# Kernel tuning notes

Measured on AMD Instinct MI355X. Metric: run time of the kernel, lower is better.

## Reference

```python
import jax, jax.numpy as jnp
import numpy as np

N_NODES = 50000
N_EDGES = 400000
D = 100  # trans_units = node_dim = edge_dim = out_dim


def setup_inputs() -> dict:
    key = jax.random.key(0)
    ks = jax.random.split(key, 8)
    x = jax.random.normal(ks[0], (N_NODES, D), dtype=jnp.float32)
    edge_h = jax.random.normal(ks[1], (N_EDGES, D), dtype=jnp.float32)
    src = jax.random.randint(ks[2], (N_EDGES,), 0, N_NODES)
    dst = jax.random.randint(ks[3], (N_EDGES,), 0, N_NODES)
    # xavier-normal-ish init scales (gain for relu ~ sqrt(2))
    W_fc = jax.random.normal(ks[4], (D, D), dtype=jnp.float32) * np.sqrt(2.0 / (D + D))
    W_rel = jax.random.normal(ks[5], (2 * D, D), dtype=jnp.float32) * np.sqrt(2.0 / (3 * D))
    b_rel = jnp.zeros((D,), dtype=jnp.float32)
    W_attn = jax.random.normal(ks[6], (2 * D, 1), dtype=jnp.float32) * np.sqrt(2.0 / (2 * D + 1))
    return {"x": x, "edge_h": edge_h, "src": src, "dst": dst,
            "W_fc": W_fc, "W_rel": W_rel, "b_rel": b_rel, "W_attn": W_attn}


def reference(x, edge_h, src, dst, W_fc, W_rel, b_rel, W_attn):
    """RGATLayer forward (single layer, single head, as in RGAT defaults).

    z = fc(x); per-edge: end = relation_fc([edge_h, z[dst]]);
    e = leaky_relu(attn_fc([z[src], end])); alpha = softmax over incoming
    edges of each dst node; h[dst] = sum alpha * z[src].
    """
    n = x.shape[0]
    z = x @ W_fc                                              # [N, D]
    z_src = z[src]                                            # [E, D]
    z_dst = z[dst]                                            # [E, D]
    end = jnp.concatenate([edge_h, z_dst], axis=-1) @ W_rel + b_rel   # [E, D]
    a = jnp.concatenate([z_src, end], axis=-1) @ W_attn              # [E, 1]
    e = jax.nn.leaky_relu(a[:, 0], negative_slope=0.01)             # [E]
    # segment softmax over edges grouped by destination node
    m = jax.ops.segment_max(e, dst, num_segments=n)                  # [N]
    ex = jnp.exp(e - m[dst])                                         # [E]
    denom = jax.ops.segment_sum(ex, dst, num_segments=n)            # [N]
    alpha = ex / denom[dst]                                          # [E]
    # weighted scatter-sum of source messages (zero-in-degree nodes -> 0)
    h = jax.ops.segment_sum(alpha[:, None] * z_src, dst, num_segments=n)  # [N, D]
    return h
```

## Files before the change

### kernel.cpp

```cpp
#include <hip/hip_runtime.h>
#include <hip/hip_bf16.h>

#define NN 50000
#define NE 400000
#define DD 100
#define CAP 32

#define OFF_P    0
#define OFF_Q    112
#define OFF_C    224
#define OFF_WB   240
#define OFF_S    7424
#define OFF_T    (OFF_S + NN)
#define OFF_CNT  (OFF_T + NN)
#define OFF_PAY  (OFF_CNT + NN + 16)
#define OFF_Z    (OFF_PAY + 2 * CAP * NN)

#define FC_ROWS 128
#define NFCB ((NN + FC_ROWS - 1) / FC_ROWS)

#define PB_FOLD 51
#define PB_ZERO 49
#define PB_WPK  4

typedef __attribute__((ext_vector_type(8))) short bf8;
typedef __attribute__((ext_vector_type(4))) float f4;

__device__ __forceinline__ unsigned pk2(float a, float b) {
    __hip_bfloat16 ha = __float2bfloat16(a), hb = __float2bfloat16(b);
    unsigned short ua, ub;
    __builtin_memcpy(&ua, &ha, 2); __builtin_memcpy(&ub, &hb, 2);
    return (unsigned)ua | ((unsigned)ub << 16);
}
__device__ __forceinline__ float bflo(unsigned u) { return __uint_as_float(u << 16); }
__device__ __forceinline__ float bfhi(unsigned u) { return __uint_as_float(u & 0xffff0000u); }

__global__ void k_prep(const float* __restrict__ W_rel, const float* __restrict__ b_rel,
                       const float* __restrict__ W_attn, const float* __restrict__ W_fc,
                       float* __restrict__ ws) {
    int b = blockIdx.x, t = threadIdx.x;
    const int lane = t & 63;
    if (b < PB_FOLD) {
        int gw = b * 4 + (t >> 6);
        if (gw < 201) {
            const float* row = (gw < 200) ? (W_rel + (size_t)gw * DD) : b_rel;
            float v0 = (lane < DD)      ? W_attn[DD + lane]      : 0.f;
            float v1 = (lane + 64 < DD) ? W_attn[DD + 64 + lane] : 0.f;
            float a0 = (lane < DD)      ? row[lane]      : 0.f;
            float a1 = (lane + 64 < DD) ? row[64 + lane] : 0.f;
            float s = fmaf(a0, v0, a1 * v1);
            #pragma unroll
            for (int m = 1; m < 64; m <<= 1) s += __shfl_xor(s, m);
            if (lane == 0) {
                if (gw < 100)      ws[OFF_P + gw] = s;
                else if (gw < 200) ws[OFF_Q + gw - 100] = s;
                else               ws[OFF_C] = s;
            }
        }
    } else if (b < PB_FOLD + PB_ZERO) {
        int* cnt = (int*)(ws + OFF_CNT);
        int i0 = (b - PB_FOLD) * 1024 + t;
        int lim = (b - PB_FOLD) * 1024 + 1024; if (lim > NN) lim = NN;
        for (int i = i0; i < lim; i += 256) cnt[i] = 0;
    } else {
        char* wbB = (char*)(ws + OFF_WB);
        int bi = b - PB_FOLD - PB_ZERO;
        for (int i = bi * 1792 + t; i < (bi + 1) * 1792; i += 256) {
            int kp = i / 112, c = i - kp * 112;
            int k = 2 * kp;
            float f0 = (c < DD && k < DD)     ? W_fc[k * DD + c]       : 0.f;
            float f1 = (c < DD && k + 1 < DD) ? W_fc[(k + 1) * DD + c] : 0.f;
            int sw = (c & 7) << 4;
            *(unsigned*)(wbB + ((c * 256 + 2 * k) ^ sw)) = pk2(f0, f1);
        }
    }
}

__launch_bounds__(256, 4)
__global__ void k_fc(const float* __restrict__ x, const float* __restrict__ W_attn,
                     float* __restrict__ ws) {
    __shared__ __align__(16) char smem[32768];
    int tid = threadIdx.x;

    int row0 = blockIdx.x * FC_ROWS;
    int nrows = NN - row0; if (nrows > FC_ROWS) nrows = FC_ROWS;

    char* xb = smem;
    const float4* x4 = reinterpret_cast<const float4*>(x + (size_t)row0 * DD);
    for (int i = tid; i < 128 * 25; i += 256) {
        int r = i / 25, k4 = i - r * 25, k = k4 * 4;
        float4 v = (r < nrows) ? x4[i] : make_float4(0.f, 0.f, 0.f, 0.f);
        int sw = (r & 7) << 4;
        *(unsigned*)(xb + ((r * 256 + 2 * k) ^ sw))     = pk2(v.x, v.y);
        *(unsigned*)(xb + ((r * 256 + 2 * k + 4) ^ sw)) = pk2(v.z, v.w);
    }
    for (int i = tid; i < 128 * 7; i += 256) {
        int r = i / 7, j = i - r * 7, k = 100 + j * 4;
        int sw = (r & 7) << 4;
        *(unsigned*)(xb + ((r * 256 + 2 * k) ^ sw)) = 0u;
        *(unsigned*)(xb + ((r * 256 + 2 * k + 4) ^ sw)) = 0u;
    }
    __syncthreads();

    const int w = tid >> 6, lane = tid & 63;
    const int lq = lane & 15, lg = lane >> 4;
    const int sw = (lq & 7) << 4;
    const char* wbG = (const char*)(ws + OFF_WB);

    f4 acc[2][7];
    #pragma unroll
    for (int mt = 0; mt < 2; ++mt)
        #pragma unroll
        for (int nt = 0; nt < 7; ++nt)
            acc[mt][nt] = (f4){0.f, 0.f, 0.f, 0.f};

    #pragma unroll
    for (int ks = 0; ks < 4; ++ks) {
        const int ko = ks * 64 + lg * 16;
        bf8 a0 = *(const bf8*)(xb + (((w * 32 + lq) * 256 + ko) ^ sw));
        bf8 a1 = *(const bf8*)(xb + (((w * 32 + 16 + lq) * 256 + ko) ^ sw));
        #pragma unroll
        for (int nt = 0; nt < 7; ++nt) {
            bf8 bfr = *(const bf8*)(wbG + (((nt * 16 + lq) * 256 + ko) ^ sw));
            acc[0][nt] = __builtin_amdgcn_mfma_f32_16x16x32_bf16(a0, bfr, acc[0][nt], 0, 0, 0);
            acc[1][nt] = __builtin_amdgcn_mfma_f32_16x16x32_bf16(a1, bfr, acc[1][nt], 0, 0, 0);
        }
    }

    float sp0[4] = {0,0,0,0}, sp1[4] = {0,0,0,0}, tp0[4] = {0,0,0,0}, tp1[4] = {0,0,0,0};
    #pragma unroll
    for (int nt = 0; nt < 7; ++nt) {
        int col = nt * 16 + lq;
        float uv = W_attn[col];
        float qv = ws[OFF_Q + col];
        #pragma unroll
        for (int r = 0; r < 4; ++r) {
            sp0[r] = fmaf(acc[0][nt][r], uv, sp0[r]);
            tp0[r] = fmaf(acc[0][nt][r], qv, tp0[r]);
            sp1[r] = fmaf(acc[1][nt][r], uv, sp1[r]);
            tp1[r] = fmaf(acc[1][nt][r], qv, tp1[r]);
        }
    }
    #pragma unroll
    for (int m = 1; m < 16; m <<= 1) {
        #pragma unroll
        for (int r = 0; r < 4; ++r) {
            sp0[r] += __shfl_xor(sp0[r], m);
            tp0[r] += __shfl_xor(tp0[r], m);
            sp1[r] += __shfl_xor(sp1[r], m);
            tp1[r] += __shfl_xor(tp1[r], m);
        }
    }
    if (lq == 0) {
        #pragma unroll
        for (int r = 0; r < 4; ++r) {
            int g0 = row0 + w * 32 + lg * 4 + r;
            int g1 = g0 + 16;
            if (g0 < NN) { ws[OFF_S + g0] = sp0[r]; ws[OFF_T + g0] = tp0[r]; }
            if (g1 < NN) { ws[OFF_S + g1] = sp1[r]; ws[OFF_T + g1] = tp1[r]; }
        }
    }

    __syncthreads();
    float* zt = (float*)smem;
    #pragma unroll
    for (int half = 0; half < 2; ++half) {
        if ((w >> 1) == half) {
            #pragma unroll
            for (int mt = 0; mt < 2; ++mt)
                #pragma unroll
                for (int nt = 0; nt < 7; ++nt) {
                    int c = nt * 16 + lq;
                    if (c < 104) {
                        int rbase = (w & 1) * 32 + mt * 16 + lg * 4;
                        #pragma unroll
                        for (int r = 0; r < 4; ++r)
                            zt[(rbase + r) * 104 + c] = acc[mt][nt][r];
                    }
                }
        }
        __syncthreads();
        int rlo = half * 64;
        int rcnt = nrows - rlo; if (rcnt > 64) rcnt = 64;
        if (rcnt > 0) {
            unsigned* zbase = (unsigned*)(ws + OFF_Z) + (size_t)(row0 + rlo) * 50;
            for (int i = tid; i < rcnt * 25; i += 256) {
                int r = i / 25, c4 = i - r * 25;
                const float* s = zt + r * 104 + c4 * 4;
                uint2 v; v.x = pk2(s[0], s[1]); v.y = pk2(s[2], s[3]);
                *reinterpret_cast<uint2*>(zbase + (size_t)r * 50 + c4 * 2) = v;
            }
        }
        __syncthreads();
    }
}

__launch_bounds__(256)
__global__ void k_edge2(const float* __restrict__ edge_h, const int* __restrict__ src,
                        const int* __restrict__ dst, float* __restrict__ ws) {
    const float* p = ws + OFF_P;
    int* cnt = (int*)(ws + OFF_CNT);
    float2* pay = reinterpret_cast<float2*>(ws + OFF_PAY);
    const float cterm = ws[OFF_C];
    const int part = threadIdx.x & 3;

    float4 pf[6];
    #pragma unroll
    for (int j = 0; j < 6; ++j)
        pf[j] = *reinterpret_cast<const float4*>(p + part * 4 + j * 16);
    const float ptail = p[96 + part];

    const int groups_per_iter = (gridDim.x * blockDim.x) >> 2;
    const int g0 = (blockIdx.x * blockDim.x + threadIdx.x) >> 2;

    for (int e = g0; e < NE; e += groups_per_iter) {
        int sn = src[e], dn = dst[e];
        int cur = 0;
        if (part == 0) cur = atomicAdd(&cnt[dn], 1);
        float sv = ws[OFF_S + sn];
        float tv = ws[OFF_T + dn];

        const float* eh = edge_h + (size_t)e * DD;
        float pd = 0.f;
        #pragma unroll
        for (int j = 0; j < 6; ++j) {
            float4 v = *reinterpret_cast<const float4*>(eh + part * 4 + j * 16);
            pd = fmaf(v.x, pf[j].x, pd);
            pd = fmaf(v.y, pf[j].y, pd);
            pd = fmaf(v.z, pf[j].z, pd);
            pd = fmaf(v.w, pf[j].w, pd);
        }
        pd = fmaf(eh[96 + part], ptail, pd);
        pd += __shfl_xor(pd, 1);
        pd += __shfl_xor(pd, 2);

        if (part == 0) {
            float a = pd + sv + tv + cterm;
            float ev = a > 0.f ? a : 0.01f * a;
            float ex = __expf(ev);
            if (cur < CAP) {
                float2 pl; pl.x = __int_as_float(sn); pl.y = ex;
                pay[(size_t)dn * CAP + cur] = pl;
            }
        }
    }
}

__launch_bounds__(256)
__global__ void k_gather(float* __restrict__ h, const float* __restrict__ ws) {
    int i = blockIdx.x * blockDim.x + threadIdx.x;
    if (i >= NN * 25) return;
    int n = i / 25;
    int c = i - n * 25;
    const int* cnt = (const int*)(ws + OFF_CNT);
    const float2* pay = reinterpret_cast<const float2*>(ws + OFF_PAY) + (size_t)n * CAP;
    const unsigned* zu = (const unsigned*)(ws + OFF_Z);

    int cn = cnt[n]; if (cn > CAP) cn = CAP;
    float4 a0 = make_float4(0.f, 0.f, 0.f, 0.f);
    float4 a1 = make_float4(0.f, 0.f, 0.f, 0.f);
    float den = 0.f;
    int j = 0;
    for (; j + 2 <= cn; j += 2) {
        float2 p0 = pay[j], p1 = pay[j + 1];
        int s0 = __float_as_int(p0.x), s1 = __float_as_int(p1.x);
        float e0 = p0.y, e1 = p1.y;
        uint2 v0 = *reinterpret_cast<const uint2*>(zu + (size_t)s0 * 50 + c * 2);
        uint2 v1 = *reinterpret_cast<const uint2*>(zu + (size_t)s1 * 50 + c * 2);
        den += e0 + e1;
        a0.x = fmaf(e0, bflo(v0.x), a0.x);
        a0.y = fmaf(e0, bfhi(v0.x), a0.y);
        a0.z = fmaf(e0, bflo(v0.y), a0.z);
        a0.w = fmaf(e0, bfhi(v0.y), a0.w);
        a1.x = fmaf(e1, bflo(v1.x), a1.x);
        a1.y = fmaf(e1, bfhi(v1.x), a1.y);
        a1.z = fmaf(e1, bflo(v1.y), a1.z);
        a1.w = fmaf(e1, bfhi(v1.y), a1.w);
    }
    if (j < cn) {
        float2 p0 = pay[j];
        int s0 = __float_as_int(p0.x);
        float e0 = p0.y;
        uint2 v0 = *reinterpret_cast<const uint2*>(zu + (size_t)s0 * 50 + c * 2);
        den += e0;
        a0.x = fmaf(e0, bflo(v0.x), a0.x);
        a0.y = fmaf(e0, bfhi(v0.x), a0.y);
        a0.z = fmaf(e0, bflo(v0.y), a0.z);
        a0.w = fmaf(e0, bfhi(v0.y), a0.w);
    }
    float inv = (den > 0.f) ? 1.0f / den : 0.f;
    float4 acc;
    acc.x = (a0.x + a1.x) * inv;
    acc.y = (a0.y + a1.y) * inv;
    acc.z = (a0.z + a1.z) * inv;
    acc.w = (a0.w + a1.w) * inv;
    *reinterpret_cast<float4*>(h + (size_t)n * DD + c * 4) = acc;
}

extern "C" void kernel_launch(void* const* d_in, const int* in_sizes, int n_in,
                              void* d_out, int out_size, void* d_ws, size_t ws_size,
                              hipStream_t stream) {
    const float* x      = (const float*)d_in[0];
    const float* edge_h = (const float*)d_in[1];
    const int*   src    = (const int*)d_in[2];
    const int*   dst    = (const int*)d_in[3];
    const float* W_fc   = (const float*)d_in[4];
    const float* W_rel  = (const float*)d_in[5];
    const float* b_rel  = (const float*)d_in[6];
    const float* W_attn = (const float*)d_in[7];
    float* h  = (float*)d_out;
    float* ws = (float*)d_ws;

    k_prep<<<PB_FOLD + PB_ZERO + PB_WPK, 256, 0, stream>>>(W_rel, b_rel, W_attn, W_fc, ws);
    k_fc<<<NFCB, 256, 0, stream>>>(x, W_attn, ws);
    k_edge2<<<2048, 256, 0, stream>>>(edge_h, src, dst, ws);
    k_gather<<<(NN * 25 + 255) / 256, 256, 0, stream>>>(h, ws);
}
```

Baseline: 85.78 us.

## Overlap edge_h dot-product with node FC in one launch, split atomic scatter

The per-edge edge_h·p dot product, which reads the large edge_h array, moves into extra blocks of the FC kernel so that streaming edge_h runs concurrently with the node MFMA transform. The scalar results are stored in a new workspace buffer. A lightweight one-thread-per-edge kernel then does the atomic slot reservation, adds the src/dst terms, applies exp and writes the payload. This aims to hide the edge_h bandwidth behind the FC compute and shrink the serial edge stage, at the cost of an extra write and read of a per-edge float.

New measurement: 95.01 us. 1.11x slower.

```diff
diff --git a/kernel.cpp b/kernel.cpp
--- a/kernel.cpp
+++ b/kernel.cpp
@@ -15,9 +15,11 @@
 #define OFF_CNT  (OFF_T + NN)
 #define OFF_PAY  (OFF_CNT + NN + 16)
 #define OFF_Z    (OFF_PAY + 2 * CAP * NN)
+#define OFF_PD   (OFF_Z + NN * 50)
 
 #define FC_ROWS 128
 #define NFCB ((NN + FC_ROWS - 1) / FC_ROWS)
+#define NMAIN 2048
 
 #define PB_FOLD 51
 #define PB_ZERO 49
@@ -77,10 +79,43 @@
 }
 
 __launch_bounds__(256, 4)
-__global__ void k_fc(const float* __restrict__ x, const float* __restrict__ W_attn,
-                     float* __restrict__ ws) {
+__global__ void k_main(const float* __restrict__ x, const float* __restrict__ edge_h,
+                       const float* __restrict__ W_attn, float* __restrict__ ws) {
     __shared__ __align__(16) char smem[32768];
     int tid = threadIdx.x;
+
+    if (blockIdx.x >= NFCB) {
+        const float* p = ws + OFF_P;
+        float* pdb = ws + OFF_PD;
+        const int part = tid & 3;
+        float4 pf[6];
+        #pragma unroll
+        for (int j = 0; j < 6; ++j)
+            pf[j] = *reinterpret_cast<const float4*>(p + part * 4 + j * 16);
+        const float ptail = p[96 + part];
+
+        const int nsb = NMAIN - NFCB;
+        const int groups_per_iter = (nsb * 256) >> 2;
+        const int g0 = ((blockIdx.x - NFCB) * 256 + tid) >> 2;
+
+        for (int e = g0; e < NE; e += groups_per_iter) {
+            const float* eh = edge_h + (size_t)e * DD;
+            float pd = 0.f;
+            #pragma unroll
+            for (int j = 0; j < 6; ++j) {
+                float4 v = *reinterpret_cast<const float4*>(eh + part * 4 + j * 16);
+                pd = fmaf(v.x, pf[j].x, pd);
+                pd = fmaf(v.y, pf[j].y, pd);
+                pd = fmaf(v.z, pf[j].z, pd);
+                pd = fmaf(v.w, pf[j].w, pd);
+            }
+            pd = fmaf(eh[96 + part], ptail, pd);
+            pd += __shfl_xor(pd, 1);
+            pd += __shfl_xor(pd, 2);
+            if (part == 0) pdb[e] = pd;
+        }
+        return;
+    }
 
     int row0 = blockIdx.x * FC_ROWS;
     int nrows = NN - row0; if (nrows > FC_ROWS) nrows = FC_ROWS;
@@ -196,53 +231,22 @@
 }
 
 __launch_bounds__(256)
-__global__ void k_edge2(const float* __restrict__ edge_h, const int* __restrict__ src,
-                        const int* __restrict__ dst, float* __restrict__ ws) {
-    const float* p = ws + OFF_P;
+__global__ void k_edge3(const int* __restrict__ src, const int* __restrict__ dst,
+                        float* __restrict__ ws) {
+    int e = blockIdx.x * 256 + threadIdx.x;
+    if (e >= NE) return;
     int* cnt = (int*)(ws + OFF_CNT);
     float2* pay = reinterpret_cast<float2*>(ws + OFF_PAY);
     const float cterm = ws[OFF_C];
-    const int part = threadIdx.x & 3;
-
-    float4 pf[6];
-    #pragma unroll
-    for (int j = 0; j < 6; ++j)
-        pf[j] = *reinterpret_cast<const float4*>(p + part * 4 + j * 16);
-    const float ptail = p[96 + part];
-
-    const int groups_per_iter = (gridDim.x * blockDim.x) >> 2;
-    const int g0 = (blockIdx.x * blockDim.x + threadIdx.x) >> 2;
-
-    for (int e = g0; e < NE; e += groups_per_iter) {
-        int sn = src[e], dn = dst[e];
-        int cur = 0;
-        if (part == 0) cur = atomicAdd(&cnt[dn], 1);
-        float sv = ws[OFF_S + sn];
-        float tv = ws[OFF_T + dn];
-
-        const float* eh = edge_h + (size_t)e * DD;
-        float pd = 0.f;
-        #pragma unroll
-        for (int j = 0; j < 6; ++j) {
-            float4 v = *reinterpret_cast<const float4*>(eh + part * 4 + j * 16);
-            pd = fmaf(v.x, pf[j].x, pd);
-            pd = fmaf(v.y, pf[j].y, pd);
-            pd = fmaf(v.z, pf[j].z, pd);
-            pd = fmaf(v.w, pf[j].w, pd);
-        }
-        pd = fmaf(eh[96 + part], ptail, pd);
-        pd += __shfl_xor(pd, 1);
-        pd += __shfl_xor(pd, 2);
-
-        if (part == 0) {
-            float a = pd + sv + tv + cterm;
-            float ev = a > 0.f ? a : 0.01f * a;
-            float ex = __expf(ev);
-            if (cur < CAP) {
-                float2 pl; pl.x = __int_as_float(sn); pl.y = ex;
-                pay[(size_t)dn * CAP + cur] = pl;
-            }
-        }
+
+    int sn = src[e], dn = dst[e];
+    int cur = atomicAdd(&cnt[dn], 1);
+    float a = ws[OFF_PD + e] + ws[OFF_S + sn] + ws[OFF_T + dn] + cterm;
+    float ev = a > 0.f ? a : 0.01f * a;
+    float ex = __expf(ev);
+    if (cur < CAP) {
+        float2 pl; pl.x = __int_as_float(sn); pl.y = ex;
+        pay[(size_t)dn * CAP + cur] = pl;
     }
 }
 
@@ -312,7 +316,7 @@
     float* ws = (float*)d_ws;
 
     k_prep<<<PB_FOLD + PB_ZERO + PB_WPK, 256, 0, stream>>>(W_rel, b_rel, W_attn, W_fc, ws);
-    k_fc<<<NFCB, 256, 0, stream>>>(x, W_attn, ws);
-    k_edge2<<<2048, 256, 0, stream>>>(edge_h, src, dst, ws);
+    k_main<<<NMAIN, 256, 0, stream>>>(x, edge_h, W_attn, ws);
+    k_edge3<<<(NE + 255) / 256, 256, 0, stream>>>(src, dst, ws);
     k_gather<<<(NN * 25 + 255) / 256, 256, 0, stream>>>(h, ws);
 }
```
